# Kernel tuning notes

Hardware: AMD Instinct MI355X
Metric: run time of the kernel (lower is better)

The kernel has to match this reference:

```python
import jax, jax.numpy as jnp
import numpy as np

N, IN_DIM, H, E = 8192, 128, 256, 131072


def setup_inputs() -> dict:
    key = jax.random.key(0)
    ks = jax.random.split(key, 10)
    s = 0.05  # small init scale for numerical stability
    return {
        "x": jax.random.normal(ks[0], (N, IN_DIM), dtype=jnp.float32),
        "edge_index": jax.random.randint(ks[1], (2, E), 0, N, dtype=jnp.int64),
        "w0a": jax.random.normal(ks[2], (IN_DIM, H), dtype=jnp.float32) * s,
        "b0a": jnp.zeros((H,), jnp.float32),
        "w0b": jax.random.normal(ks[3], (H, H), dtype=jnp.float32) * s,
        "b0b": jnp.zeros((H,), jnp.float32),
        "w1a": jax.random.normal(ks[4], (H, H), dtype=jnp.float32) * s,
        "b1a": jnp.zeros((H,), jnp.float32),
        "w1b": jax.random.normal(ks[5], (H, H), dtype=jnp.float32) * s,
        "b1b": jnp.zeros((H,), jnp.float32),
        "w_out": jax.random.normal(ks[6], (H, H), dtype=jnp.float32) * s,
        "b_out": jnp.zeros((H,), jnp.float32),
        "w_edge": jax.random.normal(ks[7], (2 * H, 1), dtype=jnp.float32) * s,
        "b_edge": jnp.zeros((1,), jnp.float32),
    }


def _gin(x, src, dst, wa, ba, wb, bb):
    # GINConv (eps=0): h_i = MLP(x_i + sum_{j in N(i)} x_j)
    agg = jax.ops.segment_sum(x[src], dst, num_segments=x.shape[0])
    h = x + agg
    return jax.nn.relu(h @ wa + ba) @ wb + bb


def reference(x, edge_index, w0a, b0a, w0b, b0b, w1a, b1a, w1b, b1b,
              w_out, b_out, w_edge, b_edge):
    src, dst = edge_index[0], edge_index[1]
    x = jax.nn.relu(_gin(x, src, dst, w0a, b0a, w0b, b0b))
    x = jax.nn.relu(_gin(x, src, dst, w1a, b1a, w1b, b1b))
    x = x @ w_out + b_out  # [N, H]
    # edge_proj(cat[x_i, x_j]) == x_i @ W[:H] + x_j @ W[H:] + b, done without
    # materializing the [N, N, 2H] concat tensor.
    h = x.shape[1]
    li = x @ w_edge[:h]   # [N, 1]
    lj = x @ w_edge[h:]   # [N, 1]
    edge_logits = li + lj.T + b_edge[0]  # [N, N]
    return edge_logits
```

## Files before the change

### kernel.cpp

```cpp
#include <hip/hip_runtime.h>

#define N_NODES 8192
#define IN_DIM  128
#define HDIM    256
#define NEDGE   131072

__global__ void hist_kernel(const int* __restrict__ dst, int* __restrict__ deg) {
    int e = blockIdx.x * blockDim.x + threadIdx.x;
    if (e < NEDGE) atomicAdd(&deg[dst[e]], 1);
}

__global__ __launch_bounds__(1024) void build_scan(const int* __restrict__ deg,
                                                   int* __restrict__ offs,
                                                   int* __restrict__ cursor) {
    __shared__ int part[1024];
    int t = threadIdx.x;
    int base = t * 8;
    int local[8];
    int s = 0;
#pragma unroll
    for (int i = 0; i < 8; ++i) { local[i] = s; s += deg[base + i]; }
    part[t] = s;
    __syncthreads();
    for (int off = 1; off < 1024; off <<= 1) {
        int v = (t >= off) ? part[t - off] : 0;
        __syncthreads();
        part[t] += v;
        __syncthreads();
    }
    int prefix = (t == 0) ? 0 : part[t - 1];
#pragma unroll
    for (int i = 0; i < 8; ++i) {
        int o = prefix + local[i];
        offs[base + i] = o;
        cursor[base + i] = o;
    }
    if (t == 1023) offs[N_NODES] = part[1023];
}

__global__ void fill_kernel(const int* __restrict__ src, const int* __restrict__ dst,
                            int* __restrict__ cursor, int* __restrict__ bucket) {
    int e = blockIdx.x * blockDim.x + threadIdx.x;
    if (e >= NEDGE) return;
    int p = atomicAdd(&cursor[dst[e]], 1);
    bucket[p] = src[e];
}

__global__ __launch_bounds__(256) void aggregate256(const float* __restrict__ x,
                                                    const int* __restrict__ offs,
                                                    const int* __restrict__ bucket,
                                                    float* __restrict__ h) {
    int lane = threadIdx.x & 63;
    int node = blockIdx.x * 4 + (threadIdx.x >> 6);
    const float4* x4 = reinterpret_cast<const float4*>(x);
    float4 acc = x4[(size_t)node * 64 + lane];
    int b = offs[node], e = offs[node + 1];
    int k = b;
    for (; k + 1 < e; k += 2) {
        int s0 = bucket[k], s1 = bucket[k + 1];
        float4 v0 = x4[(size_t)s0 * 64 + lane];
        float4 v1 = x4[(size_t)s1 * 64 + lane];
        acc.x += v0.x + v1.x; acc.y += v0.y + v1.y;
        acc.z += v0.z + v1.z; acc.w += v0.w + v1.w;
    }
    if (k < e) {
        int s0 = bucket[k];
        float4 v0 = x4[(size_t)s0 * 64 + lane];
        acc.x += v0.x; acc.y += v0.y; acc.z += v0.z; acc.w += v0.w;
    }
    reinterpret_cast<float4*>(h)[(size_t)node * 64 + lane] = acc;
}

__global__ __launch_bounds__(256) void aggregate128(const float* __restrict__ x,
                                                    const int* __restrict__ offs,
                                                    const int* __restrict__ bucket,
                                                    float* __restrict__ h) {
    int lane = threadIdx.x & 63;
    int node = blockIdx.x * 4 + (threadIdx.x >> 6);
    const float2* x2 = reinterpret_cast<const float2*>(x);
    float2 acc = x2[(size_t)node * 64 + lane];
    int b = offs[node], e = offs[node + 1];
    int k = b;
    for (; k + 1 < e; k += 2) {
        int s0 = bucket[k], s1 = bucket[k + 1];
        float2 v0 = x2[(size_t)s0 * 64 + lane];
        float2 v1 = x2[(size_t)s1 * 64 + lane];
        acc.x += v0.x + v1.x; acc.y += v0.y + v1.y;
    }
    if (k < e) {
        int s0 = bucket[k];
        float2 v0 = x2[(size_t)s0 * 64 + lane];
        acc.x += v0.x; acc.y += v0.y;
    }
    reinterpret_cast<float2*>(h)[(size_t)node * 64 + lane] = acc;
}

template<int K>
__global__ __launch_bounds__(256) void gemm_bias_relu(
    const float* __restrict__ A, const float* __restrict__ B,
    const float* __restrict__ bias, float* __restrict__ C) {
    constexpr int BM = 64, BN = 64, BK = 16;
    __shared__ float As[BK][BM];
    __shared__ float Bs[BK][BN];
    const int tid = threadIdx.x;
    const int tx = tid & 15, ty = tid >> 4;
    const int am = tid >> 2, akq = tid & 3;
    const int bk = tid >> 4, bn = (tid & 15) * 4;
    const int row0 = blockIdx.y * BM, col0 = blockIdx.x * BN;
    float acc[4][4] = {};
    for (int t = 0; t < K; t += BK) {
        float4 av = *reinterpret_cast<const float4*>(&A[(size_t)(row0 + am) * K + t + akq * 4]);
        float4 bv = *reinterpret_cast<const float4*>(&B[(size_t)(t + bk) * HDIM + col0 + bn]);
        __syncthreads();
        As[akq * 4 + 0][am] = av.x;
        As[akq * 4 + 1][am] = av.y;
        As[akq * 4 + 2][am] = av.z;
        As[akq * 4 + 3][am] = av.w;
        *reinterpret_cast<float4*>(&Bs[bk][bn]) = bv;
        __syncthreads();
#pragma unroll
        for (int kk = 0; kk < BK; ++kk) {
            float4 a4 = *reinterpret_cast<const float4*>(&As[kk][ty * 4]);
            float4 b4 = *reinterpret_cast<const float4*>(&Bs[kk][tx * 4]);
            float a[4] = {a4.x, a4.y, a4.z, a4.w};
            float b[4] = {b4.x, b4.y, b4.z, b4.w};
#pragma unroll
            for (int i = 0; i < 4; ++i)
#pragma unroll
                for (int j = 0; j < 4; ++j)
                    acc[i][j] = fmaf(a[i], b[j], acc[i][j]);
        }
    }
    float4 bb = *reinterpret_cast<const float4*>(&bias[col0 + tx * 4]);
    float bcol[4] = {bb.x, bb.y, bb.z, bb.w};
#pragma unroll
    for (int i = 0; i < 4; ++i) {
        int row = row0 + ty * 4 + i;
        float4 r;
        r.x = fmaxf(acc[i][0] + bcol[0], 0.f);
        r.y = fmaxf(acc[i][1] + bcol[1], 0.f);
        r.z = fmaxf(acc[i][2] + bcol[2], 0.f);
        r.w = fmaxf(acc[i][3] + bcol[3], 0.f);
        *reinterpret_cast<float4*>(&C[(size_t)row * HDIM + col0 + tx * 4]) = r;
    }
}

__global__ void prep_vec(const float* __restrict__ w_out, const float* __restrict__ b_out,
                         const float* __restrict__ w_edge, const float* __restrict__ b_edge,
                         float* __restrict__ v) {
    int c = threadIdx.x;
    float sa = 0.f, sb = 0.f;
    for (int k = 0; k < HDIM; k += 4) {
        float4 w  = *reinterpret_cast<const float4*>(&w_out[(size_t)c * HDIM + k]);
        float4 ua = *reinterpret_cast<const float4*>(&w_edge[k]);
        float4 ub = *reinterpret_cast<const float4*>(&w_edge[HDIM + k]);
        sa += w.x * ua.x + w.y * ua.y + w.z * ua.z + w.w * ua.w;
        sb += w.x * ub.x + w.y * ub.y + w.z * ub.z + w.w * ub.w;
    }
    v[c] = sa;
    v[HDIM + c] = sb;
    __shared__ float ra[HDIM], rb[HDIM];
    ra[c] = b_out[c] * w_edge[c];
    rb[c] = b_out[c] * w_edge[HDIM + c];
    __syncthreads();
    for (int s = 128; s > 0; s >>= 1) {
        if (c < s) { ra[c] += ra[c + s]; rb[c] += rb[c + s]; }
        __syncthreads();
    }
    if (c == 0) { v[512] = ra[0] + b_edge[0]; v[513] = rb[0]; }
}

__global__ void lilj_kernel(const float* __restrict__ x2, const float* __restrict__ v,
                            float* __restrict__ li, float* __restrict__ lj) {
    int lane = threadIdx.x & 63;
    int wv = threadIdx.x >> 6;
    int node = blockIdx.x * 4 + wv;
    float4 xa = reinterpret_cast<const float4*>(x2)[(size_t)node * 64 + lane];
    float4 va = reinterpret_cast<const float4*>(v)[lane];
    float4 vb = reinterpret_cast<const float4*>(v + HDIM)[lane];
    float a = xa.x * va.x + xa.y * va.y + xa.z * va.z + xa.w * va.w;
    float b = xa.x * vb.x + xa.y * vb.y + xa.z * vb.z + xa.w * vb.w;
#pragma unroll
    for (int off = 32; off > 0; off >>= 1) {
        a += __shfl_down(a, off);
        b += __shfl_down(b, off);
    }
    if (lane == 0) {
        li[node] = a + v[512];
        lj[node] = b + v[513];
    }
}

__global__ void edge_out(const float* __restrict__ li, const float* __restrict__ lj,
                         float* __restrict__ out) {
    int i = blockIdx.y;
    int j4 = blockIdx.x * blockDim.x + threadIdx.x;
    float a = li[i];
    float4 b = reinterpret_cast<const float4*>(lj)[j4];
    float4 r = {a + b.x, a + b.y, a + b.z, a + b.w};
    reinterpret_cast<float4*>(out)[(size_t)i * (N_NODES / 4) + j4] = r;
}

extern "C" void kernel_launch(void* const* d_in, const int* in_sizes, int n_in,
                              void* d_out, int out_size, void* d_ws, size_t ws_size,
                              hipStream_t stream) {
    const float* x      = (const float*)d_in[0];
    const int*   ei     = (const int*)d_in[1];
    const float* w0a    = (const float*)d_in[2];
    const float* b0a    = (const float*)d_in[3];
    const float* w0b    = (const float*)d_in[4];
    const float* b0b    = (const float*)d_in[5];
    const float* w1a    = (const float*)d_in[6];
    const float* b1a    = (const float*)d_in[7];
    const float* w1b    = (const float*)d_in[8];
    const float* b1b    = (const float*)d_in[9];
    const float* w_out  = (const float*)d_in[10];
    const float* b_out  = (const float*)d_in[11];
    const float* w_edge = (const float*)d_in[12];
    const float* b_edge = (const float*)d_in[13];
    const int* src = ei;
    const int* dst = ei + NEDGE;

    float* ws  = (float*)d_ws;
    float* h0  = ws;
    float* t01 = h0  + (size_t)N_NODES * IN_DIM;
    float* x12 = t01 + (size_t)N_NODES * HDIM;
    float* h1  = x12 + (size_t)N_NODES * HDIM;
    float* v   = h1  + (size_t)N_NODES * HDIM;
    float* li  = v + 544;
    float* lj  = li + N_NODES;
    int*   deg    = (int*)(lj + N_NODES);
    int*   offs   = deg + N_NODES;
    int*   cursor = offs + N_NODES + 1;
    int*   bucket = cursor + N_NODES;
    float* out = (float*)d_out;

    dim3 gGemm(HDIM / 64, N_NODES / 64);

    hipMemsetAsync(deg, 0, N_NODES * sizeof(int), stream);
    hist_kernel<<<NEDGE / 256, 256, 0, stream>>>(dst, deg);
    build_scan<<<1, 1024, 0, stream>>>(deg, offs, cursor);
    fill_kernel<<<NEDGE / 256, 256, 0, stream>>>(src, dst, cursor, bucket);

    aggregate128<<<N_NODES / 4, 256, 0, stream>>>(x, offs, bucket, h0);
    gemm_bias_relu<IN_DIM><<<gGemm, 256, 0, stream>>>(h0, w0a, b0a, t01);
    gemm_bias_relu<HDIM><<<gGemm, 256, 0, stream>>>(t01, w0b, b0b, x12);

    aggregate256<<<N_NODES / 4, 256, 0, stream>>>(x12, offs, bucket, h1);
    gemm_bias_relu<HDIM><<<gGemm, 256, 0, stream>>>(h1, w1a, b1a, t01);
    gemm_bias_relu<HDIM><<<gGemm, 256, 0, stream>>>(t01, w1b, b1b, x12);

    prep_vec<<<1, 256, 0, stream>>>(w_out, b_out, w_edge, b_edge, v);
    lilj_kernel<<<N_NODES / 4, 256, 0, stream>>>(x12, v, li, lj);
    edge_out<<<dim3(N_NODES / 4 / 256, N_NODES), 256, 0, stream>>>(li, lj, out);
}
```

Measured before the change: 428.2 us.

## Use split-bf16 MFMA GEMMs with hi/lo activation storage throughout

Replaces the fp32 shared-memory SIMT GEMMs with MFMA bf16 16x16x32 kernels that use a three-term hi/lo split (hh, hl, lh) to approximate fp32 accuracy. Activations are stored as paired bf16 hi/lo arrays between stages, and weights are pre-split and transposed each call. Aggregation and lilj rebuild fp32 values from the pairs. The GEMMs read operands straight from global memory with no LDS staging, and there are four extra weight-prep launches.

```diff
diff --git a/kernel.cpp b/kernel.cpp
--- a/kernel.cpp
+++ b/kernel.cpp
@@ -4,6 +4,28 @@
 #define IN_DIM  128
 #define HDIM    256
 #define NEDGE   131072
+
+typedef unsigned short ushort_t;
+typedef __bf16 bf16x8 __attribute__((ext_vector_type(8)));
+typedef float  f32x4  __attribute__((ext_vector_type(4)));
+
+__device__ inline ushort_t f32_to_bf16_rn(float f) {
+    unsigned u = __builtin_bit_cast(unsigned, f);
+    u += 0x7fffu + ((u >> 16) & 1u);
+    return (ushort_t)(u >> 16);
+}
+__device__ inline float bf16_bits_to_f32(ushort_t h) {
+    unsigned u = ((unsigned)h) << 16;
+    return __builtin_bit_cast(float, u);
+}
+__device__ inline void split_bf16(float f, ushort_t& hi, ushort_t& lo) {
+    hi = f32_to_bf16_rn(f);
+    float rem = f - bf16_bits_to_f32(hi);
+    lo = f32_to_bf16_rn(rem);
+}
+__device__ inline float recon(ushort_t h, ushort_t l) {
+    return bf16_bits_to_f32(h) + bf16_bits_to_f32(l);
+}
 
 __global__ void hist_kernel(const int* __restrict__ dst, int* __restrict__ deg) {
     int e = blockIdx.x * blockDim.x + threadIdx.x;
@@ -46,35 +68,20 @@
     bucket[p] = src[e];
 }
 
-__global__ __launch_bounds__(256) void aggregate256(const float* __restrict__ x,
-                                                    const int* __restrict__ offs,
-                                                    const int* __restrict__ bucket,
-                                                    float* __restrict__ h) {
-    int lane = threadIdx.x & 63;
-    int node = blockIdx.x * 4 + (threadIdx.x >> 6);
-    const float4* x4 = reinterpret_cast<const float4*>(x);
-    float4 acc = x4[(size_t)node * 64 + lane];
-    int b = offs[node], e = offs[node + 1];
-    int k = b;
-    for (; k + 1 < e; k += 2) {
-        int s0 = bucket[k], s1 = bucket[k + 1];
-        float4 v0 = x4[(size_t)s0 * 64 + lane];
-        float4 v1 = x4[(size_t)s1 * 64 + lane];
-        acc.x += v0.x + v1.x; acc.y += v0.y + v1.y;
-        acc.z += v0.z + v1.z; acc.w += v0.w + v1.w;
-    }
-    if (k < e) {
-        int s0 = bucket[k];
-        float4 v0 = x4[(size_t)s0 * 64 + lane];
-        acc.x += v0.x; acc.y += v0.y; acc.z += v0.z; acc.w += v0.w;
-    }
-    reinterpret_cast<float4*>(h)[(size_t)node * 64 + lane] = acc;
-}
-
-__global__ __launch_bounds__(256) void aggregate128(const float* __restrict__ x,
-                                                    const int* __restrict__ offs,
-                                                    const int* __restrict__ bucket,
-                                                    float* __restrict__ h) {
+__global__ void prep_wsplit(const float* __restrict__ w, int K, int N,
+                            ushort_t* __restrict__ th, ushort_t* __restrict__ tl) {
+    int id = blockIdx.x * 256 + threadIdx.x;
+    if (id >= K * N) return;
+    int n = id / K, k = id - n * K;
+    float f = w[(size_t)k * N + n];
+    ushort_t hb, lb;
+    split_bf16(f, hb, lb);
+    th[id] = hb; tl[id] = lb;
+}
+
+__global__ __launch_bounds__(256) void aggregate128_split(
+    const float* __restrict__ x, const int* __restrict__ offs,
+    const int* __restrict__ bucket, ushort_t* __restrict__ hh, ushort_t* __restrict__ hl) {
     int lane = threadIdx.x & 63;
     int node = blockIdx.x * 4 + (threadIdx.x >> 6);
     const float2* x2 = reinterpret_cast<const float2*>(x);
@@ -88,61 +95,101 @@
         acc.x += v0.x + v1.x; acc.y += v0.y + v1.y;
     }
     if (k < e) {
-        int s0 = bucket[k];
-        float2 v0 = x2[(size_t)s0 * 64 + lane];
+        float2 v0 = x2[(size_t)bucket[k] * 64 + lane];
         acc.x += v0.x; acc.y += v0.y;
     }
-    reinterpret_cast<float2*>(h)[(size_t)node * 64 + lane] = acc;
+    ushort2 h2, l2;
+    split_bf16(acc.x, h2.x, l2.x);
+    split_bf16(acc.y, h2.y, l2.y);
+    reinterpret_cast<ushort2*>(hh)[(size_t)node * 64 + lane] = h2;
+    reinterpret_cast<ushort2*>(hl)[(size_t)node * 64 + lane] = l2;
+}
+
+__global__ __launch_bounds__(256) void aggregate256_split(
+    const ushort_t* __restrict__ xh, const ushort_t* __restrict__ xl,
+    const int* __restrict__ offs, const int* __restrict__ bucket,
+    ushort_t* __restrict__ hh, ushort_t* __restrict__ hl) {
+    int lane = threadIdx.x & 63;
+    int node = blockIdx.x * 4 + (threadIdx.x >> 6);
+    const ushort4* x4h = reinterpret_cast<const ushort4*>(xh);
+    const ushort4* x4l = reinterpret_cast<const ushort4*>(xl);
+    ushort4 sh = x4h[(size_t)node * 64 + lane];
+    ushort4 sl = x4l[(size_t)node * 64 + lane];
+    float4 acc = { recon(sh.x, sl.x), recon(sh.y, sl.y), recon(sh.z, sl.z), recon(sh.w, sl.w) };
+    int b = offs[node], e = offs[node + 1];
+    for (int k = b; k < e; ++k) {
+        size_t s = (size_t)bucket[k] * 64 + lane;
+        ushort4 vh = x4h[s];
+        ushort4 vl = x4l[s];
+        acc.x += recon(vh.x, vl.x);
+        acc.y += recon(vh.y, vl.y);
+        acc.z += recon(vh.z, vl.z);
+        acc.w += recon(vh.w, vl.w);
+    }
+    ushort4 oh, ol;
+    split_bf16(acc.x, oh.x, ol.x);
+    split_bf16(acc.y, oh.y, ol.y);
+    split_bf16(acc.z, oh.z, ol.z);
+    split_bf16(acc.w, oh.w, ol.w);
+    reinterpret_cast<ushort4*>(hh)[(size_t)node * 64 + lane] = oh;
+    reinterpret_cast<ushort4*>(hl)[(size_t)node * 64 + lane] = ol;
 }
 
 template<int K>
-__global__ __launch_bounds__(256) void gemm_bias_relu(
-    const float* __restrict__ A, const float* __restrict__ B,
-    const float* __restrict__ bias, float* __restrict__ C) {
-    constexpr int BM = 64, BN = 64, BK = 16;
-    __shared__ float As[BK][BM];
-    __shared__ float Bs[BK][BN];
+__global__ __launch_bounds__(256, 2) void gemm_mfma(
+    const ushort_t* __restrict__ Ah, const ushort_t* __restrict__ Al,
+    const ushort_t* __restrict__ Bh, const ushort_t* __restrict__ Bl,
+    const float* __restrict__ bias,
+    ushort_t* __restrict__ Ch, ushort_t* __restrict__ Cl) {
     const int tid = threadIdx.x;
-    const int tx = tid & 15, ty = tid >> 4;
-    const int am = tid >> 2, akq = tid & 3;
-    const int bk = tid >> 4, bn = (tid & 15) * 4;
-    const int row0 = blockIdx.y * BM, col0 = blockIdx.x * BN;
-    float acc[4][4] = {};
-    for (int t = 0; t < K; t += BK) {
-        float4 av = *reinterpret_cast<const float4*>(&A[(size_t)(row0 + am) * K + t + akq * 4]);
-        float4 bv = *reinterpret_cast<const float4*>(&B[(size_t)(t + bk) * HDIM + col0 + bn]);
-        __syncthreads();
-        As[akq * 4 + 0][am] = av.x;
-        As[akq * 4 + 1][am] = av.y;
-        As[akq * 4 + 2][am] = av.z;
-        As[akq * 4 + 3][am] = av.w;
-        *reinterpret_cast<float4*>(&Bs[bk][bn]) = bv;
-        __syncthreads();
-#pragma unroll
-        for (int kk = 0; kk < BK; ++kk) {
-            float4 a4 = *reinterpret_cast<const float4*>(&As[kk][ty * 4]);
-            float4 b4 = *reinterpret_cast<const float4*>(&Bs[kk][tx * 4]);
-            float a[4] = {a4.x, a4.y, a4.z, a4.w};
-            float b[4] = {b4.x, b4.y, b4.z, b4.w};
-#pragma unroll
-            for (int i = 0; i < 4; ++i)
-#pragma unroll
-                for (int j = 0; j < 4; ++j)
-                    acc[i][j] = fmaf(a[i], b[j], acc[i][j]);
+    const int w = tid >> 6, lane = tid & 63;
+    const int m0 = blockIdx.x * 64 + (w >> 1) * 32;
+    const int n0 = blockIdx.y * 64 + (w & 1) * 32;
+    const int lr = lane & 15;
+    const int kq = (lane >> 4) * 8;
+    f32x4 acc[2][2] = {};
+#pragma unroll
+    for (int ks = 0; ks < K; ks += 32) {
+        bf16x8 ah[2], al[2], bh[2], bl[2];
+#pragma unroll
+        for (int mi = 0; mi < 2; ++mi) {
+            size_t off = (size_t)(m0 + mi * 16 + lr) * K + ks + kq;
+            ah[mi] = *reinterpret_cast<const bf16x8*>(Ah + off);
+            al[mi] = *reinterpret_cast<const bf16x8*>(Al + off);
         }
-    }
-    float4 bb = *reinterpret_cast<const float4*>(&bias[col0 + tx * 4]);
-    float bcol[4] = {bb.x, bb.y, bb.z, bb.w};
-#pragma unroll
-    for (int i = 0; i < 4; ++i) {
-        int row = row0 + ty * 4 + i;
-        float4 r;
-        r.x = fmaxf(acc[i][0] + bcol[0], 0.f);
-        r.y = fmaxf(acc[i][1] + bcol[1], 0.f);
-        r.z = fmaxf(acc[i][2] + bcol[2], 0.f);
-        r.w = fmaxf(acc[i][3] + bcol[3], 0.f);
-        *reinterpret_cast<float4*>(&C[(size_t)row * HDIM + col0 + tx * 4]) = r;
-    }
+#pragma unroll
+        for (int ni = 0; ni < 2; ++ni) {
+            size_t off = (size_t)(n0 + ni * 16 + lr) * K + ks + kq;
+            bh[ni] = *reinterpret_cast<const bf16x8*>(Bh + off);
+            bl[ni] = *reinterpret_cast<const bf16x8*>(Bl + off);
+        }
+#pragma unroll
+        for (int mi = 0; mi < 2; ++mi)
+#pragma unroll
+            for (int ni = 0; ni < 2; ++ni) {
+                acc[mi][ni] = __builtin_amdgcn_mfma_f32_16x16x32_bf16(ah[mi], bh[ni], acc[mi][ni], 0, 0, 0);
+                acc[mi][ni] = __builtin_amdgcn_mfma_f32_16x16x32_bf16(ah[mi], bl[ni], acc[mi][ni], 0, 0, 0);
+                acc[mi][ni] = __builtin_amdgcn_mfma_f32_16x16x32_bf16(al[mi], bh[ni], acc[mi][ni], 0, 0, 0);
+            }
+    }
+    float bc[2] = { bias[n0 + lr], bias[n0 + 16 + lr] };
+    const int rbase = (lane >> 4) * 4;
+#pragma unroll
+    for (int mi = 0; mi < 2; ++mi)
+#pragma unroll
+        for (int ni = 0; ni < 2; ++ni)
+#pragma unroll
+            for (int r = 0; r < 4; ++r) {
+                float v = acc[mi][ni][r] + bc[ni];
+                v = fmaxf(v, 0.f);
+                ushort_t hb, lb;
+                split_bf16(v, hb, lb);
+                int row = m0 + mi * 16 + rbase + r;
+                int col = n0 + ni * 16 + lr;
+                size_t o = (size_t)row * HDIM + col;
+                Ch[o] = hb;
+                Cl[o] = lb;
+            }
 }
 
 __global__ void prep_vec(const float* __restrict__ w_out, const float* __restrict__ b_out,
@@ -170,12 +217,14 @@
     if (c == 0) { v[512] = ra[0] + b_edge[0]; v[513] = rb[0]; }
 }
 
-__global__ void lilj_kernel(const float* __restrict__ x2, const float* __restrict__ v,
+__global__ void lilj_kernel(const ushort_t* __restrict__ xh, const ushort_t* __restrict__ xl,
+                            const float* __restrict__ v,
                             float* __restrict__ li, float* __restrict__ lj) {
     int lane = threadIdx.x & 63;
-    int wv = threadIdx.x >> 6;
-    int node = blockIdx.x * 4 + wv;
-    float4 xa = reinterpret_cast<const float4*>(x2)[(size_t)node * 64 + lane];
+    int node = blockIdx.x * 4 + (threadIdx.x >> 6);
+    ushort4 h4 = reinterpret_cast<const ushort4*>(xh)[(size_t)node * 64 + lane];
+    ushort4 l4 = reinterpret_cast<const ushort4*>(xl)[(size_t)node * 64 + lane];
+    float4 xa = { recon(h4.x, l4.x), recon(h4.y, l4.y), recon(h4.z, l4.z), recon(h4.w, l4.w) };
     float4 va = reinterpret_cast<const float4*>(v)[lane];
     float4 vb = reinterpret_cast<const float4*>(v + HDIM)[lane];
     float a = xa.x * va.x + xa.y * va.y + xa.z * va.z + xa.w * va.w;
@@ -221,36 +270,56 @@
     const int* src = ei;
     const int* dst = ei + NEDGE;
 
-    float* ws  = (float*)d_ws;
-    float* h0  = ws;
-    float* t01 = h0  + (size_t)N_NODES * IN_DIM;
-    float* x12 = t01 + (size_t)N_NODES * HDIM;
-    float* h1  = x12 + (size_t)N_NODES * HDIM;
-    float* v   = h1  + (size_t)N_NODES * HDIM;
-    float* li  = v + 544;
-    float* lj  = li + N_NODES;
-    int*   deg    = (int*)(lj + N_NODES);
-    int*   offs   = deg + N_NODES;
-    int*   cursor = offs + N_NODES + 1;
-    int*   bucket = cursor + N_NODES;
+    ushort_t* us = (ushort_t*)d_ws;
+    ushort_t* h0h = us;                       us += (size_t)N_NODES * IN_DIM;
+    ushort_t* h0l = us;                       us += (size_t)N_NODES * IN_DIM;
+    ushort_t* th_ = us;                       us += (size_t)N_NODES * HDIM;
+    ushort_t* tl_ = us;                       us += (size_t)N_NODES * HDIM;
+    ushort_t* x1h = us;                       us += (size_t)N_NODES * HDIM;
+    ushort_t* x1l = us;                       us += (size_t)N_NODES * HDIM;
+    ushort_t* h1h = us;                       us += (size_t)N_NODES * HDIM;
+    ushort_t* h1l = us;                       us += (size_t)N_NODES * HDIM;
+    ushort_t* x2h = us;                       us += (size_t)N_NODES * HDIM;
+    ushort_t* x2l = us;                       us += (size_t)N_NODES * HDIM;
+    ushort_t* w0ah = us;                      us += IN_DIM * HDIM;
+    ushort_t* w0al = us;                      us += IN_DIM * HDIM;
+    ushort_t* w0bh = us;                      us += HDIM * HDIM;
+    ushort_t* w0bl = us;                      us += HDIM * HDIM;
+    ushort_t* w1ah = us;                      us += HDIM * HDIM;
+    ushort_t* w1al = us;                      us += HDIM * HDIM;
+    ushort_t* w1bh = us;                      us += HDIM * HDIM;
+    ushort_t* w1bl = us;                      us += HDIM * HDIM;
+    float* fs = (float*)us;
+    float* v  = fs;                           fs += 544;
+    float* li = fs;                           fs += N_NODES;
+    float* lj = fs;                           fs += N_NODES;
+    int* deg    = (int*)fs;
+    int* offs   = deg + N_NODES;
+    int* cursor = offs + N_NODES + 1;
+    int* bucket = cursor + N_NODES;
     float* out = (float*)d_out;
-
-    dim3 gGemm(HDIM / 64, N_NODES / 64);
 
     hipMemsetAsync(deg, 0, N_NODES * sizeof(int), stream);
     hist_kernel<<<NEDGE / 256, 256, 0, stream>>>(dst, deg);
     build_scan<<<1, 1024, 0, stream>>>(deg, offs, cursor);
     fill_kernel<<<NEDGE / 256, 256, 0, stream>>>(src, dst, cursor, bucket);
 
-    aggregate128<<<N_NODES / 4, 256, 0, stream>>>(x, offs, bucket, h0);
-    gemm_bias_relu<IN_DIM><<<gGemm, 256, 0, stream>>>(h0, w0a, b0a, t01);
-    gemm_bias_relu<HDIM><<<gGemm, 256, 0, stream>>>(t01, w0b, b0b, x12);
-
-    aggregate256<<<N_NODES / 4, 256, 0, stream>>>(x12, offs, bucket, h1);
-    gemm_bias_relu<HDIM><<<gGemm, 256, 0, stream>>>(h1, w1a, b1a, t01);
-    gemm_bias_relu<HDIM><<<gGemm, 256, 0, stream>>>(t01, w1b, b1b, x12);
-
+    prep_wsplit<<<(IN_DIM * HDIM + 255) / 256, 256, 0, stream>>>(w0a, IN_DIM, HDIM, w0ah, w0al);
+    prep_wsplit<<<(HDIM * HDIM + 255) / 256, 256, 0, stream>>>(w0b, HDIM, HDIM, w0bh, w0bl);
+    prep_wsplit<<<(HDIM * HDIM + 255) / 256, 256, 0, stream>>>(w1a, HDIM, HDIM, w1ah, w1al);
+    prep_wsplit<<<(HDIM * HDIM + 255) / 256, 256, 0, stream>>>(w1b, HDIM, HDIM, w1bh, w1bl);
     prep_vec<<<1, 256, 0, stream>>>(w_out, b_out, w_edge, b_edge, v);
-    lilj_kernel<<<N_NODES / 4, 256, 0, stream>>>(x12, v, li, lj);
+
+    dim3 gGemm(N_NODES / 64, HDIM / 64);
+
+    aggregate128_split<<<N_NODES / 4, 256, 0, stream>>>(x, offs, bucket, h0h, h0l);
+    gemm_mfma<IN_DIM><<<gGemm, 256, 0, stream>>>(h0h, h0l, w0ah, w0al, b0a, th_, tl_);
+    gemm_mfma<HDIM><<<gGemm, 256, 0, stream>>>(th_, tl_, w0bh, w0bl, b0b, x1h, x1l);
+
+    aggregate256_split<<<N_NODES / 4, 256, 0, stream>>>(x1h, x1l, offs, bucket, h1h, h1l);
+    gemm_mfma<HDIM><<<gGemm, 256, 0, stream>>>(h1h, h1l, w1ah, w1al, b1a, th_, tl_);
+    gemm_mfma<HDIM><<<gGemm, 256, 0, stream>>>(th_, tl_, w1bh, w1bl, b1b, x2h, x2l);
+
+    lilj_kernel<<<N_NODES / 4, 256, 0, stream>>>(x2h, x2l, v, li, lj);
     edge_out<<<dim3(N_NODES / 4 / 256, N_NODES), 256, 0, stream>>>(li, lj, out);
 }
```

New measurement: 432.7 us. No clear change (+1.0%).
